# Optimization experiments

Hardware: AMD Instinct MI355X
Metric: run time of the kernel (lower is better)

The kernel has to match this reference:

```python
import jax, jax.numpy as jnp
import numpy as np

N = 100_000      # nodes
E = 1_600_000    # edges (before self-loops)
IN, OUT, HID = 64, 32, 64
BN_EPS = 1e-5

def _mlp(h, w1, b1, g, beta, w2, b2):
    # PyG MLP (num_layers=2, plain_last=True): Linear -> BatchNorm(train) -> ReLU -> Linear
    h = h @ w1 + b1
    mu = jnp.mean(h, axis=0)
    var = jnp.var(h, axis=0)
    h = (h - mu) * jax.lax.rsqrt(var + BN_EPS) * g + beta
    return jax.nn.relu(h) @ w2 + b2

def setup_inputs() -> dict:
    key = jax.random.key(0)
    ks = jax.random.split(key, 12)
    def rn(k, shape):
        fan_in = shape[0]
        return jax.random.normal(k, shape, jnp.float32) / np.sqrt(fan_in)
    x = jax.random.normal(ks[0], (N, IN), jnp.float32)
    pos = jax.random.normal(ks[1], (N, 3), jnp.float32)
    edge_index = jax.random.randint(ks[2], (2, E), 0, N, jnp.int64)
    return {
        "x": x, "pos": pos, "edge_index": edge_index,
        "w_lin": rn(ks[3], (IN, OUT)), "w_src": rn(ks[4], (IN, OUT)), "w_dst": rn(ks[5], (IN, OUT)),
        "pos_w1": rn(ks[6], (3, HID)), "pos_b1": jnp.zeros((HID,), jnp.float32),
        "pos_g": jnp.ones((HID,), jnp.float32), "pos_beta": jnp.zeros((HID,), jnp.float32),
        "pos_w2": rn(ks[7], (HID, OUT)), "pos_b2": jnp.zeros((OUT,), jnp.float32),
        "att_w1": rn(ks[8], (OUT, HID)), "att_b1": jnp.zeros((HID,), jnp.float32),
        "att_g": jnp.ones((HID,), jnp.float32), "att_beta": jnp.zeros((HID,), jnp.float32),
        "att_w2": rn(ks[9], (HID, OUT)), "att_b2": jnp.zeros((OUT,), jnp.float32),
    }

def reference(x, pos, edge_index, w_lin, w_src, w_dst,
              pos_w1, pos_b1, pos_g, pos_beta, pos_w2, pos_b2,
              att_w1, att_b1, att_g, att_beta, att_w2, att_b2):
    n = x.shape[0]
    # add self-loops (PointTransformerConv default add_self_loops=True)
    loops = jnp.arange(n, dtype=edge_index.dtype)
    src = jnp.concatenate([edge_index[0], loops])  # j (message source)
    dst = jnp.concatenate([edge_index[1], loops])  # i (message target)

    alpha_src = x @ w_src          # [N, OUT]
    alpha_dst = x @ w_dst          # [N, OUT]
    x_val = x @ w_lin              # [N, OUT]

    delta = _mlp(pos[dst] - pos[src], pos_w1, pos_b1, pos_g, pos_beta, pos_w2, pos_b2)  # [E', OUT]
    a = _mlp(alpha_dst[dst] - alpha_src[src] + delta, att_w1, att_b1, att_g, att_beta, att_w2, att_b2)

    # per-destination-node, per-channel softmax over incoming edges
    a_max = jax.ops.segment_max(a, dst, num_segments=n)           # [N, OUT]
    a = jnp.exp(a - a_max[dst])
    denom = jax.ops.segment_sum(a, dst, num_segments=n)           # [N, OUT]
    a = a / (denom[dst] + 1e-16)

    msg = a * (x_val[src] + delta)                                # [E', OUT]
    out = jax.ops.segment_sum(msg, dst, num_segments=n)           # [N, OUT]
    return out
```

## Files before the change

kernel.cpp:

```cpp
#include <hip/hip_runtime.h>

typedef unsigned int uint;
typedef unsigned short ushort;

#define BN_EPS 1e-5f

using bf16x8 = __attribute__((ext_vector_type(8))) short;
using f32x16 = __attribute__((ext_vector_type(16))) float;

union FragU { uint w[4]; bf16x8 v; };

__device__ __forceinline__ uint pk2(float lo, float hi) {
    uint r;
    asm("v_cvt_pk_bf16_f32 %0, %1, %2" : "=v"(r) : "v"(lo), "v"(hi));
    return r;
}
__device__ __forceinline__ float bfu_lo(uint u) { return __uint_as_float(u << 16); }
__device__ __forceinline__ float bfu_hi(uint u) { return __uint_as_float(u & 0xffff0000u); }

__device__ __forceinline__ void get_rowmap(int col, int* rowv) {
    FragU pa, pb;
    float c = (float)col;
    #pragma unroll
    for (int j = 0; j < 4; j++) { pa.w[j] = pk2(c, c); pb.w[j] = pk2(1.f, 1.f); }
    f32x16 d;
    #pragma unroll
    for (int r = 0; r < 16; r++) d[r] = 0.f;
    d = __builtin_amdgcn_mfma_f32_32x32x16_bf16(pa.v, pb.v, d, 0, 0, 0);
    #pragma unroll
    for (int r = 0; r < 16; r++) {
        int m = (int)(d[r] * 0.0625f + 0.5f);
        rowv[r] = (m < 0) ? 0 : (m > 31 ? 31 : m);
    }
}

template<bool SORTED>
__device__ __forceinline__ void edge_sd(int e, const int* __restrict__ ei,
                                        const int* __restrict__ srcs,
                                        const int* __restrict__ dsts,
                                        int nE, int& src, int& dst) {
    if (SORTED) { src = srcs[e]; dst = dsts[e]; }
    else if (e < nE) { src = ei[e]; dst = ei[nE + e]; }
    else { src = e - nE; dst = src; }
}

__global__ __launch_bounds__(256) void k_node_lin(
    const float* __restrict__ x,
    const float* __restrict__ w_src, const float* __restrict__ w_dst,
    const float* __restrict__ w_lin,
    uint* __restrict__ aSb, uint* __restrict__ aDb, uint* __restrict__ xvb,
    int nNodes)
{
    int n = blockIdx.x * 256 + threadIdx.x;
    if (n >= nNodes) return;
    float xr[64];
    const float4* xp = (const float4*)(x + (size_t)n * 64);
    #pragma unroll
    for (int i = 0; i < 16; i++) {
        float4 v = xp[i];
        xr[4*i] = v.x; xr[4*i+1] = v.y; xr[4*i+2] = v.z; xr[4*i+3] = v.w;
    }
    const float* ws[3] = { w_src, w_dst, w_lin };
    uint* outs[3] = { aSb, aDb, xvb };
    #pragma unroll
    for (int m = 0; m < 3; m++) {
        const float* w = ws[m];
        float acc[32];
        #pragma unroll
        for (int o = 0; o < 32; o++) acc[o] = 0.f;
        #pragma unroll
        for (int k = 0; k < 64; k++) {
            float xk = xr[k];
            #pragma unroll
            for (int o = 0; o < 32; o++) acc[o] = fmaf(xk, w[k*32+o], acc[o]);
        }
        uint4* op = (uint4*)(outs[m] + (size_t)n * 16);
        #pragma unroll
        for (int q = 0; q < 4; q++) {
            uint4 v;
            v.x = pk2(acc[8*q+0], acc[8*q+1]);
            v.y = pk2(acc[8*q+2], acc[8*q+3]);
            v.z = pk2(acc[8*q+4], acc[8*q+5]);
            v.w = pk2(acc[8*q+6], acc[8*q+7]);
            op[q] = v;
        }
    }
}

__global__ __launch_bounds__(256) void k_pos4(
    const float* __restrict__ pos, float4* __restrict__ pos4, int n)
{
    int i = blockIdx.x * 256 + threadIdx.x;
    if (i < n) pos4[i] = make_float4(pos[i*3], pos[i*3+1], pos[i*3+2], 0.f);
}

__global__ __launch_bounds__(256) void k_hist(
    const int* __restrict__ ei, int* __restrict__ cnt, int nE, int eTot)
{
    int e = blockIdx.x * 256 + threadIdx.x;
    if (e >= eTot) return;
    int dst = (e < nE) ? ei[nE + e] : (e - nE);
    atomicAdd(&cnt[dst], 1);
}

#define SCH 1024
__global__ __launch_bounds__(256) void k_scan1(
    const int* __restrict__ cnt, int* __restrict__ cur,
    int* __restrict__ blkS, int n)
{
    __shared__ int ls[256];
    int t = threadIdx.x;
    int base = blockIdx.x * SCH + t * 4;
    int v0 = (base+0 < n) ? cnt[base+0] : 0;
    int v1 = (base+1 < n) ? cnt[base+1] : 0;
    int v2 = (base+2 < n) ? cnt[base+2] : 0;
    int v3 = (base+3 < n) ? cnt[base+3] : 0;
    int tsum = v0 + v1 + v2 + v3;
    ls[t] = tsum;
    __syncthreads();
    for (int o = 1; o < 256; o <<= 1) {
        int x = (t >= o) ? ls[t-o] : 0;
        __syncthreads();
        ls[t] += x;
        __syncthreads();
    }
    if (t == 255) blkS[blockIdx.x] = ls[255];
// ... 74 lines not shown
        partM[blockIdx.x * 9 + threadIdx.x] =
            red[0][threadIdx.x] + red[1][threadIdx.x] + red[2][threadIdx.x] + red[3][threadIdx.x];
}

__global__ void k_bn1_mom(const float* __restrict__ partM, int nBlk,
                          const float* __restrict__ pw1, const float* __restrict__ pb1,
                          const float* __restrict__ g, const float* __restrict__ beta,
                          float* __restrict__ bn, float invE)
{
    __shared__ float mom_s[9];
    int l = threadIdx.x;
    #pragma unroll
    for (int c = 0; c < 9; c++) {
        float s = 0.f;
        for (int i = l; i < nBlk; i += 64) s += partM[i*9 + c];
        for (int o = 32; o > 0; o >>= 1) s += __shfl_down(s, o, 64);
        if (l == 0) mom_s[c] = s;
    }
    __syncthreads();
    int c = l;
    if (c < 64) {
        float w0 = pw1[c], w1 = pw1[64+c], w2 = pw1[128+c], b = pb1[c];
        float S = fmaf(w0, mom_s[0], fmaf(w1, mom_s[1], w2 * mom_s[2]));
        float Q = w0*w0*mom_s[3] + 2.f*w0*w1*mom_s[4] + 2.f*w0*w2*mom_s[5]
                + w1*w1*mom_s[6] + 2.f*w1*w2*mom_s[7] + w2*w2*mom_s[8];
        float mu  = S * invE + b;
        float E2  = Q * invE + 2.f * b * (S * invE) + b * b;
        float var = fmaxf(E2 - mu * mu, 0.f);
        float sc  = rsqrtf(var + BN_EPS) * g[c];
        bn[c]      = sc;
        bn[64+c]   = beta[c] - mu * sc;
    }
}

__global__ __launch_bounds__(256) void k_red_stats(
    const float* __restrict__ partD, float* __restrict__ stats2, int nBlk)
{
    int c = blockIdx.x;
    float s = 0.f;
    for (int i = threadIdx.x; i < nBlk; i += 256) s += partD[(size_t)i*128 + c];
    for (int o = 32; o > 0; o >>= 1) s += __shfl_down(s, o, 64);
    __shared__ float red[4];
    if ((threadIdx.x & 63) == 0) red[threadIdx.x >> 6] = s;
    __syncthreads();
    if (threadIdx.x == 0) stats2[c] = red[0] + red[1] + red[2] + red[3];
}

__global__ void k_bn_fin(const float* __restrict__ stats,
                         const float* __restrict__ g, const float* __restrict__ beta,
                         const float* __restrict__ bias,
                         float* __restrict__ bn, float inv_ep)
{
    int c = threadIdx.x;
    if (c < 64) {
        float b   = bias ? bias[c] : 0.f;
        float m0  = stats[c] * inv_ep;
        float mu  = m0 + b;
        float eq  = stats[64+c] * inv_ep + 2.f*b*m0 + b*b;
        float var = fmaxf(eq - mu * mu, 0.f);
        float sc  = rsqrtf(var + BN_EPS) * g[c];
        bn[c]      = sc;
        bn[64+c]   = beta[c] - mu * sc;
    }
}

__global__ void k_fold1(const float* __restrict__ pw1, const float* __restrict__ pb1,
                        const float* __restrict__ bn1,
                        float* __restrict__ pw1f, float* __restrict__ pb1f)
{
    int i = threadIdx.x;
    if (i < 192) pw1f[i] = pw1[i] * bn1[i & 63];
    if (i < 64)  pb1f[i] = pb1[i] * bn1[i] + bn1[64 + i];
}

__global__ void k_fold2(const float* __restrict__ aw1, const float* __restrict__ ab1,
                        const float* __restrict__ bn2,
                        float* __restrict__ aw1f, float* __restrict__ ab1f)
{
    int i = blockIdx.x * 256 + threadIdx.x;
    if (i < 2048) aw1f[i] = aw1[i] * bn2[i & 63];
    if (i < 64)   ab1f[i] = ab1[i] * bn2[i] + bn2[64 + i];
}

__device__ __forceinline__ void gather_row16(
    const uint* __restrict__ rowp, const int* q2, bool quadOK,
    const int* rowv, float* out)
{
    if (quadOK) {
        #pragma unroll
        for (int g = 0; g < 4; g++) {
            uint2 v = *(const uint2*)(rowp + 2*q2[g]);
            out[4*g+0] = bfu_lo(v.x);
            out[4*g+1] = bfu_hi(v.x);
            out[4*g+2] = bfu_lo(v.y);
            out[4*g+3] = bfu_hi(v.y);
        }
    } else {
        const ushort* rp = (const ushort*)rowp;
        #pragma unroll
        for (int r = 0; r < 16; r++)
            out[r] = __uint_as_float(((uint)rp[rowv[r]]) << 16);
    }
}

template<bool SORTED>
__global__ __launch_bounds__(256, 2) void k_delta_stats(
    const int* __restrict__ ei, const int* __restrict__ srcs, const int* __restrict__ dsts,
    const float4* __restrict__ pos4,
    const uint* __restrict__ aSb, const uint* __restrict__ aDb,
    const float* __restrict__ pw1f, const float* __restrict__ pb1f,
    const float* __restrict__ pw2, const float* __restrict__ pb2,
    const float* __restrict__ aw1,
    float* __restrict__ partD, int nE, int eTot)
{
    const int lane = threadIdx.x & 63;
    const int col  = lane & 31;
    const int h    = lane >> 5;

    __shared__ float redS[4][64], redQ[4][64];
    {
        int w = threadIdx.x >> 6, c = threadIdx.x & 63;
        redS[w][c] = 0.f; redQ[w][c] = 0.f;
    }

    int rowv[16];
    get_rowmap(col, rowv);
    bool quadOK = true;
    #pragma unroll
    for (int g = 0; g < 4; g++)
        quadOK = quadOK && (rowv[4*g+1] == rowv[4*g]+1)
                        && (rowv[4*g+2] == rowv[4*g]+2)
                        && (rowv[4*g+3] == rowv[4*g]+3);
    int q2[4];
    #pragma unroll
    for (int g = 0; g < 4; g++) q2[g] = rowv[4*g] >> 2;

    FragU fw_pw2[4];
    #pragma unroll
    for (int kt = 0; kt < 4; kt++)
        #pragma unroll
        for (int jw = 0; jw < 4; jw++) {
            int m = 2*jw;
            int c0 = 16*kt + 8*(m>>2) + 4*h + (m&3);
            fw_pw2[kt].w[jw] = pk2(pw2[c0*32 + col], pw2[(c0+1)*32 + col]);
        }
    FragU fw_aw1[2][2];
    #pragma unroll
    for (int mt = 0; mt < 2; mt++)
        #pragma unroll
        for (int kt = 0; kt < 2; kt++)
            #pragma unroll
            for (int jw = 0; jw < 4; jw++) {
                int u0 = rowv[8*kt + 2*jw], u1 = rowv[8*kt + 2*jw + 1];
                fw_aw1[mt][kt].w[jw] = pk2(aw1[u0*64 + 32*mt + col],
                                           aw1[u1*64 + 32*mt + col]);
            }
    float pb2v[16];
    #pragma unroll
    for (int r = 0; r < 16; r++) pb2v[r] = pb2[rowv[r]];

    float sA[32], qA[32];
    #pragma unroll
    for (int i = 0; i < 32; i++) { sA[i] = 0.f; qA[i] = 0.f; }

    const int nT = (eTot + 31) >> 5;
    const int gw = (blockIdx.x << 2) + (threadIdx.x >> 6);
    const int nW = gridDim.x << 2;
    for (int t = gw; t < nT; t += nW) {
        int e = t*32 + col;
        bool valid = e < eTot;
        int ec = valid ? e : eTot - 1;
        int src, dst;
        edge_sd<SORTED>(ec, ei, srcs, dsts, nE, src, dst);
        float4 pd = pos4[dst], ps = pos4[src];
        float p0 = pd.x - ps.x, p1 = pd.y - ps.y, p2 = pd.z - ps.z;

        FragU ft[4];
        #pragma unroll
        for (int kt = 0; kt < 4; kt++)
            #pragma unroll
            for (int mm = 0; mm < 2; mm++) {
                int cb = 16*kt + 8*mm + 4*h;
                float4 w0 = *(const float4*)(pw1f +       cb);
                float4 w1 = *(const float4*)(pw1f + 64  + cb);
                float4 w2 = *(const float4*)(pw1f + 128 + cb);
                float4 bb = *(const float4*)(pb1f + cb);
                float t0 = fmaxf(fmaf(p0,w0.x, fmaf(p1,w1.x, fmaf(p2,w2.x, bb.x))), 0.f);
                float t1 = fmaxf(fmaf(p0,w0.y, fmaf(p1,w1.y, fmaf(p2,w2.y, bb.y))), 0.f);
                float t2 = fmaxf(fmaf(p0,w0.z, fmaf(p1,w1.z, fmaf(p2,w2.z, bb.z))), 0.f);
                float t3 = fmaxf(fmaf(p0,w0.w, fmaf(p1,w1.w, fmaf(p2,w2.w, bb.w))), 0.f);
                ft[kt].w[2*mm+0] = pk2(t0, t1);
                ft[kt].w[2*mm+1] = pk2(t2, t3);
            }
        f32x16 adl;
        #pragma unroll
        for (int r = 0; r < 16; r++) adl[r] = pb2v[r];
        #pragma unroll
        for (int kt = 0; kt < 4; kt++)
            adl = __builtin_amdgcn_mfma_f32_32x32x16_bf16(fw_pw2[kt].v, ft[kt].v, adl, 0, 0, 0);

        float gD[16], gS[16];
        gather_row16(aDb + (size_t)dst*16, q2, quadOK, rowv, gD);
        gather_row16(aSb + (size_t)src*16, q2, quadOK, rowv, gS);

        FragU fu[2];
        #pragma unroll
        for (int kt = 0; kt < 2; kt++)
            #pragma unroll
            for (int jw = 0; jw < 4; jw++) {
                int r0 = 8*kt + 2*jw;
                fu[kt].w[jw] = pk2(adl[r0]   + gD[r0]   - gS[r0],
                                   adl[r0+1] + gD[r0+1] - gS[r0+1]);
            }

        f32x16 ah0, ah1;
        #pragma unroll
        for (int r = 0; r < 16; r++) { ah0[r] = 0.f; ah1[r] = 0.f; }
        #pragma unroll
        for (int kt = 0; kt < 2; kt++) {
            ah0 = __builtin_amdgcn_mfma_f32_32x32x16_bf16(fw_aw1[0][kt].v, fu[kt].v, ah0, 0, 0, 0);
            ah1 = __builtin_amdgcn_mfma_f32_32x32x16_bf16(fw_aw1[1][kt].v, fu[kt].v, ah1, 0, 0, 0);
        }
        if (valid) {
            #pragma unroll
            for (int r = 0; r < 16; r++) {
                sA[r]    += ah0[r];
                qA[r]     = fmaf(ah0[r], ah0[r], qA[r]);
                sA[16+r] += ah1[r];
                qA[16+r]  = fmaf(ah1[r], ah1[r], qA[16+r]);
            }
        }
    }
    __syncthreads();
    {
        int w = threadIdx.x >> 6;
        #pragma unroll
        for (int idx = 0; idx < 32; idx++) {
            float vs = sA[idx], vq = qA[idx];
            for (int off = 16; off > 0; off >>= 1) {
                vs += __shfl_xor(vs, off, 64);
                vq += __shfl_xor(vq, off, 64);
            }
            if ((threadIdx.x & 31) == 0) {
                int mt = idx >> 4, r = idx & 15;
                int c = 32*mt + rowv[r];
                redS[w][c] = vs;
                redQ[w][c] = vq;
            }
        }
    }
    __syncthreads();
    if (threadIdx.x < 64) {
        int c = threadIdx.x;
        float S = redS[0][c] + redS[1][c] + redS[2][c] + redS[3][c];
        float Q = redQ[0][c] + redQ[1][c] + redQ[2][c] + redQ[3][c];
        partD[(size_t)blockIdx.x*128 + c]      = S;
        partD[(size_t)blockIdx.x*128 + 64 + c] = Q;
    }
}

template<bool SORTED>
__global__ __launch_bounds__(256, 2) void k_att_agg(
    const int* __restrict__ ei, const int* __restrict__ srcs, const int* __restrict__ dsts,
    const float4* __restrict__ pos4,
    const uint* __restrict__ aSb, const uint* __restrict__ aDb,
    const uint* __restrict__ xvb,
    const float* __restrict__ pw1f, const float* __restrict__ pb1f,
    const float* __restrict__ pw2, const float* __restrict__ pb2,
    const float* __restrict__ aw1f, const float* __restrict__ ab1f,
    const float* __restrict__ aw2, const float* __restrict__ ab2,
    float* __restrict__ denom, float* __restrict__ outp,
    int nE, int eTot)
{
    const int lane = threadIdx.x & 63;
    const int col  = lane & 31;
    const int h    = lane >> 5;

    int rowv[16];
    get_rowmap(col, rowv);
    bool quadOK = true;
    #pragma unroll
    for (int g = 0; g < 4; g++)
        quadOK = quadOK && (rowv[4*g+1] == rowv[4*g]+1)
                        && (rowv[4*g+2] == rowv[4*g]+2)
                        && (rowv[4*g+3] == rowv[4*g]+3);
    int q2[4];
    #pragma unroll
    for (int g = 0; g < 4; g++) q2[g] = rowv[4*g] >> 2;

    FragU fw_pw2[4], fw_aw2[4];
    #pragma unroll
    for (int kt = 0; kt < 4; kt++)
        #pragma unroll
        for (int jw = 0; jw < 4; jw++) {
            int m = 2*jw;
            int c0 = 16*kt + 8*(m>>2) + 4*h + (m&3);
            fw_pw2[kt].w[jw] = pk2(pw2[c0*32 + col], pw2[(c0+1)*32 + col]);
            int o0 = 32*(kt>>1) + rowv[8*(kt&1) + m];
            int o1 = 32*(kt>>1) + rowv[8*(kt&1) + m + 1];
            fw_aw2[kt].w[jw] = pk2(aw2[o0*32 + col], aw2[o1*32 + col]);
        }
    FragU fw_aw1[2][2];
    #pragma unroll
    for (int mt = 0; mt < 2; mt++)
        #pragma unroll
        for (int kt = 0; kt < 2; kt++)
            #pragma unroll
            for (int jw = 0; jw < 4; jw++) {
                int u0 = rowv[8*kt + 2*jw], u1 = rowv[8*kt + 2*jw + 1];
                fw_aw1[mt][kt].w[jw] = pk2(aw1f[u0*64 + 32*mt + col],
                                           aw1f[u1*64 + 32*mt + col]);
            }
    float pb2v[16], ab2v[16], ab1v[32];
    #pragma unroll
    for (int r = 0; r < 16; r++) {
        pb2v[r]    = pb2[rowv[r]];
        ab2v[r]    = ab2[rowv[r]];
        ab1v[r]    = ab1f[rowv[r]];
        ab1v[16+r] = ab1f[32 + rowv[r]];
    }

    const int nT = (eTot + 31) >> 5;
    const int gw = (blockIdx.x << 2) + (threadIdx.x >> 6);
    const int nW = gridDim.x << 2;
    for (int t = gw; t < nT; t += nW) {
        int e = t*32 + col;
        bool valid = e < eTot;
        int ec = valid ? e : eTot - 1;
        int src, dst;
        edge_sd<SORTED>(ec, ei, srcs, dsts, nE, src, dst);
        float4 pd = pos4[dst], ps = pos4[src];
        float p0 = pd.x - ps.x, p1 = pd.y - ps.y, p2 = pd.z - ps.z;

        FragU ft[4];
        #pragma unroll
        for (int kt = 0; kt < 4; kt++)
            #pragma unroll
            for (int mm = 0; mm < 2; mm++) {
                int cb = 16*kt + 8*mm + 4*h;
                float4 w0 = *(const float4*)(pw1f +       cb);
                float4 w1 = *(const float4*)(pw1f + 64  + cb);
                float4 w2 = *(const float4*)(pw1f + 128 + cb);
                float4 bb = *(const float4*)(pb1f + cb);
                float t0 = fmaxf(fmaf(p0,w0.x, fmaf(p1,w1.x, fmaf(p2,w2.x, bb.x))), 0.f);
                float t1 = fmaxf(fmaf(p0,w0.y, fmaf(p1,w1.y, fmaf(p2,w2.y, bb.y))), 0.f);
                float t2 = fmaxf(fmaf(p0,w0.z, fmaf(p1,w1.z, fmaf(p2,w2.z, bb.z))), 0.f);
                float t3 = fmaxf(fmaf(p0,w0.w, fmaf(p1,w1.w, fmaf(p2,w2.w, bb.w))), 0.f);
                ft[kt].w[2*mm+0] = pk2(t0, t1);
                ft[kt].w[2*mm+1] = pk2(t2, t3);
            }
        f32x16 adl;
        #pragma unroll
        for (int r = 0; r < 16; r++) adl[r] = pb2v[r];
        #pragma unroll
        for (int kt = 0; kt < 4; kt++)
            adl = __builtin_amdgcn_mfma_f32_32x32x16_bf16(fw_pw2[kt].v, ft[kt].v, adl, 0, 0, 0);

        float gD[16], gS[16], xg[16];
        gather_row16(aDb + (size_t)dst*16, q2, quadOK, rowv, gD);
        gather_row16(aSb + (size_t)src*16, q2, quadOK, rowv, gS);
        gather_row16(xvb + (size_t)src*16, q2, quadOK, rowv, xg);

        FragU fu[2];
        #pragma unroll
        for (int kt = 0; kt < 2; kt++)
            #pragma unroll
            for (int jw = 0; jw < 4; jw++) {
                int r0 = 8*kt + 2*jw;
                fu[kt].w[jw] = pk2(adl[r0]   + gD[r0]   - gS[r0],
                                   adl[r0+1] + gD[r0+1] - gS[r0+1]);
            }

        f32x16 ah0, ah1;
        #pragma unroll
        for (int r = 0; r < 16; r++) { ah0[r] = ab1v[r]; ah1[r] = ab1v[16+r]; }
        #pragma unroll
        for (int kt = 0; kt < 2; kt++) {
            ah0 = __builtin_amdgcn_mfma_f32_32x32x16_bf16(fw_aw1[0][kt].v, fu[kt].v, ah0, 0, 0, 0);
            ah1 = __builtin_amdgcn_mfma_f32_32x32x16_bf16(fw_aw1[1][kt].v, fu[kt].v, ah1, 0, 0, 0);
        }
        FragU fh[4];
        #pragma unroll
        for (int q = 0; q < 4; q++)
            #pragma unroll
            for (int jw = 0; jw < 4; jw++) {
                int r0 = 8*(q&1) + 2*jw;
                float x0 = (q < 2) ? ah0[r0]   : ah1[r0];
                float x1 = (q < 2) ? ah0[r0+1] : ah1[r0+1];
                fh[q].w[jw] = pk2(fmaxf(x0, 0.f), fmaxf(x1, 0.f));
            }
        f32x16 aa;
        #pragma unroll
        for (int r = 0; r < 16; r++) aa[r] = ab2v[r];
        aa = __builtin_amdgcn_mfma_f32_32x32x16_bf16(fw_aw2[0].v, fh[0].v, aa, 0, 0, 0);
        aa = __builtin_amdgcn_mfma_f32_32x32x16_bf16(fw_aw2[1].v, fh[1].v, aa, 0, 0, 0);
        aa = __builtin_amdgcn_mfma_f32_32x32x16_bf16(fw_aw2[2].v, fh[2].v, aa, 0, 0, 0);
        aa = __builtin_amdgcn_mfma_f32_32x32x16_bf16(fw_aw2[3].v, fh[3].v, aa, 0, 0, 0);

        if (SORTED) {
            float eav[16], msv[16];
            #pragma unroll
            for (int r = 0; r < 16; r++) {
                float ea = __expf(fminf(aa[r], 35.f));
                eav[r] = valid ? ea : 0.f;
                msv[r] = valid ? ea * (xg[r] + adl[r]) : 0.f;
            }
            int lw = lane & 31;
            int dprev = __shfl_up(dst, 1, 32);
            bool isHead = (lw == 0) || (dprev != dst);
            bool eq1  = (__shfl_down(dst, 1, 32)  == dst) && (lw + 1  < 32);
            bool eq2  = (__shfl_down(dst, 2, 32)  == dst) && (lw + 2  < 32);
            bool eq4  = (__shfl_down(dst, 4, 32)  == dst) && (lw + 4  < 32);
            bool eq8  = (__shfl_down(dst, 8, 32)  == dst) && (lw + 8  < 32);
            bool eq16 = (__shfl_down(dst, 16, 32) == dst) && (lw + 16 < 32);
            float* drow = denom + (size_t)dst * 32;
            float* orow = outp  + (size_t)dst * 32;
            #pragma unroll
            for (int r = 0; r < 16; r++) {
                float ev = eav[r], mv = msv[r];
                { float a = __shfl_down(ev,1,32),  b = __shfl_down(mv,1,32);  if (eq1)  { ev += a; mv += b; } }
                { float a = __shfl_down(ev,2,32),  b = __shfl_down(mv,2,32);  if (eq2)  { ev += a; mv += b; } }
                { float a = __shfl_down(ev,4,32),  b = __shfl_down(mv,4,32);  if (eq4)  { ev += a; mv += b; } }
                { float a = __shfl_down(ev,8,32),  b = __shfl_down(mv,8,32);  if (eq8)  { ev += a; mv += b; } }
                { float a = __shfl_down(ev,16,32), b = __shfl_down(mv,16,32); if (eq16) { ev += a; mv += b; } }
                if (isHead) {
                    int o = rowv[r];
                    unsafeAtomicAdd(drow + o, ev);
                    unsafeAtomicAdd(orow + o, mv);
                }
            }
        } else if (valid) {
            float* drow = denom + (size_t)dst * 32;
            float* orow = outp  + (size_t)dst * 32;
            #pragma unroll
            for (int r = 0; r < 16; r++) {
                int o = rowv[r];
                float ea = __expf(fminf(aa[r], 35.f));
                unsafeAtomicAdd(drow + o, ea);
                unsafeAtomicAdd(orow + o, ea * (xg[r] + adl[r]));
            }
        }
    }
}

__global__ __launch_bounds__(256) void k_norm(
    float* __restrict__ out, const float* __restrict__ denom, int total)
{
    int i = blockIdx.x * 256 + threadIdx.x;
    if (i < total) out[i] = out[i] / (denom[i] + 1e-16f);
}

extern "C" void kernel_launch(void* const* d_in, const int* in_sizes, int n_in,
                              void* d_out, int out_size, void* d_ws, size_t ws_size,
                              hipStream_t stream)
{
    const float* x     = (const float*)d_in[0];
    const float* pos   = (const float*)d_in[1];
    const int*   ei    = (const int*)d_in[2];
    const float* w_lin = (const float*)d_in[3];
    const float* w_src = (const float*)d_in[4];
    const float* w_dst = (const float*)d_in[5];
    const float* pw1   = (const float*)d_in[6];
    const float* pb1   = (const float*)d_in[7];
    const float* pg    = (const float*)d_in[8];
    const float* pbeta = (const float*)d_in[9];
    const float* pw2   = (const float*)d_in[10];
    const float* pb2   = (const float*)d_in[11];
    const float* aw1   = (const float*)d_in[12];
    const float* ab1   = (const float*)d_in[13];
    const float* ag    = (const float*)d_in[14];
    const float* abeta = (const float*)d_in[15];
    const float* aw2   = (const float*)d_in[16];
    const float* ab2   = (const float*)d_in[17];
    float* out = (float*)d_out;

    const int nNodes = in_sizes[0] / 64;
    const int nE     = in_sizes[2] / 2;
    const int eTot   = nE + nNodes;

    const int PMBLK = 1024;
    const int DBLK  = 2048;

    const size_t nF = (size_t)nNodes * 32;
    uint*   aSb   = (uint*)d_ws;
    uint*   aDb   = aSb + (size_t)nNodes*16;
    uint*   xvb   = aDb + (size_t)nNodes*16;
    float*  pos4  = (float*)(xvb + (size_t)nNodes*16);
    float*  denom = pos4 + (size_t)nNodes*4;
    float*  stats = denom + nF;
    float*  bn1   = stats + 512;
    float*  bn2   = bn1 + 128;
    float*  pw1f  = bn2 + 128;
    float*  pb1f  = pw1f + 192;
    float*  aw1f  = pb1f + 64;
    float*  ab1f  = aw1f + 2048;
    float*  partM = ab1f + 64;
    float*  partD = partM + (size_t)PMBLK*9;
    float*  fend  = partD + (size_t)DBLK*128;

    int* cnt    = (int*)fend;
    int* cur    = cnt + nNodes;
    int* blkS   = cur + nNodes;
    int* blkOff = blkS + 256;
    int* srcs   = blkOff + 256;
    int* dsts   = srcs + eTot;

    size_t need_sorted = ((char*)(dsts + eTot)) - ((char*)d_ws);
    const bool sorted = ws_size >= need_sorted;

    const int nb = (nNodes + SCH - 1) / SCH;

    hipMemsetAsync(out,   0, nF * sizeof(float), stream);
    hipMemsetAsync(denom, 0, nF * sizeof(float), stream);

    k_node_lin<<<(nNodes + 255) / 256, 256, 0, stream>>>(
        x, w_src, w_dst, w_lin, aSb, aDb, xvb, nNodes);
    k_pos4<<<(nNodes + 255) / 256, 256, 0, stream>>>(pos, (float4*)pos4, nNodes);

    k_pos_mom<<<PMBLK, 256, 0, stream>>>(ei, (const float4*)pos4, partM, nE);
    k_bn1_mom<<<1, 64, 0, stream>>>(partM, PMBLK, pw1, pb1, pg, pbeta, bn1,
                                    1.0f / (float)eTot);
    k_fold1<<<1, 256, 0, stream>>>(pw1, pb1, bn1, pw1f, pb1f);
// ... 32 lines not shown
```

Before: 839.9 us.

## Software-prefetch next edge tile's indices and gathers in edge kernels

```diff
diff --git a/kernel.cpp b/kernel.cpp
--- a/kernel.cpp
+++ b/kernel.cpp
@@ -42,6 +42,60 @@
     if (SORTED) { src = srcs[e]; dst = dsts[e]; }
     else if (e < nE) { src = ei[e]; dst = ei[nE + e]; }
     else { src = e - nE; dst = src; }
+}
+
+__device__ __forceinline__ void unpack8(const uint2* gq, float* out) {
+    #pragma unroll
+    for (int g = 0; g < 4; g++) {
+        out[4*g+0] = bfu_lo(gq[g].x);
+        out[4*g+1] = bfu_hi(gq[g].x);
+        out[4*g+2] = bfu_lo(gq[g].y);
+        out[4*g+3] = bfu_hi(gq[g].y);
+    }
+}
+
+template<bool SORTED, bool WANTX>
+__device__ __forceinline__ void pref_tile(
+    int t, int col, int nE, int eTot,
+    const int* __restrict__ ei, const int* __restrict__ srcs, const int* __restrict__ dsts,
+    const float4* __restrict__ pos4,
+    const uint* __restrict__ aSb, const uint* __restrict__ xvb, const int* q2,
+    int& src, int& dst, float4& ps, float4& pd, uint2* gs, uint2* gx)
+{
+    int e = t*32 + col;
+    int ec = (e < eTot) ? e : eTot - 1;
+    edge_sd<SORTED>(ec, ei, srcs, dsts, nE, src, dst);
+    ps = pos4[src];
+    pd = pos4[dst];
+    const uint* rs = aSb + (size_t)src*16;
+    #pragma unroll
+    for (int g = 0; g < 4; g++) gs[g] = *(const uint2*)(rs + 2*q2[g]);
+    if (WANTX) {
+        const uint* rx = xvb + (size_t)src*16;
+        #pragma unroll
+        for (int g = 0; g < 4; g++) gx[g] = *(const uint2*)(rx + 2*q2[g]);
+    }
+}
+
+__device__ __forceinline__ void gather_row16(
+    const uint* __restrict__ rowp, const int* q2, bool quadOK,
+    const int* rowv, float* out)
+{
+    if (quadOK) {
+        #pragma unroll
+        for (int g = 0; g < 4; g++) {
+            uint2 v = *(const uint2*)(rowp + 2*q2[g]);
+            out[4*g+0] = bfu_lo(v.x);
+            out[4*g+1] = bfu_hi(v.x);
+            out[4*g+2] = bfu_lo(v.y);
+            out[4*g+3] = bfu_hi(v.y);
+        }
+    } else {
+        const ushort* rp = (const ushort*)rowp;
+        #pragma unroll
+        for (int r = 0; r < 16; r++)
+            out[r] = __uint_as_float(((uint)rp[rowv[r]]) << 16);
+    }
 }
 
 __global__ __launch_bounds__(256) void k_node_lin(
@@ -282,27 +336,6 @@
     if (i < 64)   ab1f[i] = ab1[i] * bn2[i] + bn2[64 + i];
 }
 
-__device__ __forceinline__ void gather_row16(
-    const uint* __restrict__ rowp, const int* q2, bool quadOK,
-    const int* rowv, float* out)
-{
-    if (quadOK) {
-        #pragma unroll
-        for (int g = 0; g < 4; g++) {
-            uint2 v = *(const uint2*)(rowp + 2*q2[g]);
-            out[4*g+0] = bfu_lo(v.x);
-            out[4*g+1] = bfu_hi(v.x);
-            out[4*g+2] = bfu_lo(v.y);
-            out[4*g+3] = bfu_hi(v.y);
-        }
-    } else {
-        const ushort* rp = (const ushort*)rowp;
-        #pragma unroll
-        for (int r = 0; r < 16; r++)
-            out[r] = __uint_as_float(((uint)rp[rowv[r]]) << 16);
-    }
-}
-
 template<bool SORTED>
 __global__ __launch_bounds__(256, 2) void k_delta_stats(
     const int* __restrict__ ei, const int* __restrict__ srcs, const int* __restrict__ dsts,
@@ -366,71 +399,152 @@
     const int nT = (eTot + 31) >> 5;
     const int gw = (blockIdx.x << 2) + (threadIdx.x >> 6);
     const int nW = gridDim.x << 2;
-    for (int t = gw; t < nT; t += nW) {
-        int e = t*32 + col;
-        bool valid = e < eTot;
-        int ec = valid ? e : eTot - 1;
-        int src, dst;
-        edge_sd<SORTED>(ec, ei, srcs, dsts, nE, src, dst);
-        float4 pd = pos4[dst], ps = pos4[src];
-        float p0 = pd.x - ps.x, p1 = pd.y - ps.y, p2 = pd.z - ps.z;
-
-        FragU ft[4];
-        #pragma unroll
-        for (int kt = 0; kt < 4; kt++)
-            #pragma unroll
-            for (int mm = 0; mm < 2; mm++) {
-                int cb = 16*kt + 8*mm + 4*h;
-                float4 w0 = *(const float4*)(pw1f +       cb);
-                float4 w1 = *(const float4*)(pw1f + 64  + cb);
-                float4 w2 = *(const float4*)(pw1f + 128 + cb);
-                float4 bb = *(const float4*)(pb1f + cb);
-                float t0 = fmaxf(fmaf(p0,w0.x, fmaf(p1,w1.x, fmaf(p2,w2.x, bb.x))), 0.f);
-                float t1 = fmaxf(fmaf(p0,w0.y, fmaf(p1,w1.y, fmaf(p2,w2.y, bb.y))), 0.f);
-                float t2 = fmaxf(fmaf(p0,w0.z, fmaf(p1,w1.z, fmaf(p2,w2.z, bb.z))), 0.f);
-                float t3 = fmaxf(fmaf(p0,w0.w, fmaf(p1,w1.w, fmaf(p2,w2.w, bb.w))), 0.f);
-                ft[kt].w[2*mm+0] = pk2(t0, t1);
-                ft[kt].w[2*mm+1] = pk2(t2, t3);
-            }
-        f32x16 adl;
-        #pragma unroll
-        for (int r = 0; r < 16; r++) adl[r] = pb2v[r];
-        #pragma unroll
-        for (int kt = 0; kt < 4; kt++)
-            adl = __builtin_amdgcn_mfma_f32_32x32x16_bf16(fw_pw2[kt].v, ft[kt].v, adl, 0, 0, 0);
-
-        float gD[16], gS[16];
-        gather_row16(aDb + (size_t)dst*16, q2, quadOK, rowv, gD);
-        gather_row16(aSb + (size_t)src*16, q2, quadOK, rowv, gS);
-
-        FragU fu[2];
-        #pragma unroll
-        for (int kt = 0; kt < 2; kt++)
-            #pragma unroll
-            for (int jw = 0; jw < 4; jw++) {
-                int r0 = 8*kt + 2*jw;
-                fu[kt].w[jw] = pk2(adl[r0]   + gD[r0]   - gS[r0],
-                                   adl[r0+1] + gD[r0+1] - gS[r0+1]);
-            }
-
-        f32x16 ah0, ah1;
-        #pragma unroll
-        for (int r = 0; r < 16; r++) { ah0[r] = 0.f; ah1[r] = 0.f; }
-        #pragma unroll
-        for (int kt = 0; kt < 2; kt++) {
-            ah0 = __builtin_amdgcn_mfma_f32_32x32x16_bf16(fw_aw1[0][kt].v, fu[kt].v, ah0, 0, 0, 0);
-            ah1 = __builtin_amdgcn_mfma_f32_32x32x16_bf16(fw_aw1[1][kt].v, fu[kt].v, ah1, 0, 0, 0);
+
+    if (quadOK) {
+        int c_src, c_dst; float4 c_ps, c_pd; uint2 c_gs[4], c_gx[4];
+        int t = gw;
+        if (t < nT)
+            pref_tile<SORTED, false>(t, col, nE, eTot, ei, srcs, dsts, pos4,
+                                     aSb, nullptr, q2, c_src, c_dst, c_ps, c_pd, c_gs, c_gx);
+        for (; t < nT; ) {
+            int tn = t + nW;
+            int tc = (tn < nT) ? tn : t;
+            int n_src, n_dst; float4 n_ps, n_pd; uint2 n_gs[4], n_gx[4];
+            pref_tile<SORTED, false>(tc, col, nE, eTot, ei, srcs, dsts, pos4,
+                                     aSb, nullptr, q2, n_src, n_dst, n_ps, n_pd, n_gs, n_gx);
+            bool valid = (t*32 + col) < eTot;
+            uint2 gd2[4];
+            {
+                const uint* rd = aDb + (size_t)c_dst*16;
+                #pragma unroll
+                for (int g = 0; g < 4; g++) gd2[g] = *(const uint2*)(rd + 2*q2[g]);
+            }
+            float p0 = c_pd.x - c_ps.x, p1 = c_pd.y - c_ps.y, p2 = c_pd.z - c_ps.z;
+
+            FragU ft[4];
+            #pragma unroll
+            for (int kt = 0; kt < 4; kt++)
+                #pragma unroll
+                for (int mm = 0; mm < 2; mm++) {
+                    int cb = 16*kt + 8*mm + 4*h;
+                    float4 w0 = *(const float4*)(pw1f +       cb);
+                    float4 w1 = *(const float4*)(pw1f + 64  + cb);
+                    float4 w2 = *(const float4*)(pw1f + 128 + cb);
+                    float4 bb = *(const float4*)(pb1f + cb);
+                    float t0 = fmaxf(fmaf(p0,w0.x, fmaf(p1,w1.x, fmaf(p2,w2.x, bb.x))), 0.f);
+                    float t1 = fmaxf(fmaf(p0,w0.y, fmaf(p1,w1.y, fmaf(p2,w2.y, bb.y))), 0.f);
+                    float t2 = fmaxf(fmaf(p0,w0.z, fmaf(p1,w1.z, fmaf(p2,w2.z, bb.z))), 0.f);
+                    float t3 = fmaxf(fmaf(p0,w0.w, fmaf(p1,w1.w, fmaf(p2,w2.w, bb.w))), 0.f);
+                    ft[kt].w[2*mm+0] = pk2(t0, t1);
+                    ft[kt].w[2*mm+1] = pk2(t2, t3);
+                }
+            f32x16 adl;
+            #pragma unroll
+            for (int r = 0; r < 16; r++) adl[r] = pb2v[r];
+            #pragma unroll
+            for (int kt = 0; kt < 4; kt++)
+                adl = __builtin_amdgcn_mfma_f32_32x32x16_bf16(fw_pw2[kt].v, ft[kt].v, adl, 0, 0, 0);
+
+            float gD[16], gS[16];
+            unpack8(gd2, gD);
+            unpack8(c_gs, gS);
+
+            FragU fu[2];
+            #pragma unroll
+            for (int kt = 0; kt < 2; kt++)
+                #pragma unroll
+                for (int jw = 0; jw < 4; jw++) {
+                    int r0 = 8*kt + 2*jw;
+                    fu[kt].w[jw] = pk2(adl[r0]   + gD[r0]   - gS[r0],
+                                       adl[r0+1] + gD[r0+1] - gS[r0+1]);
+                }
+
+            f32x16 ah0, ah1;
+            #pragma unroll
+            for (int r = 0; r < 16; r++) { ah0[r] = 0.f; ah1[r] = 0.f; }
+            #pragma unroll
+            for (int kt = 0; kt < 2; kt++) {
+                ah0 = __builtin_amdgcn_mfma_f32_32x32x16_bf16(fw_aw1[0][kt].v, fu[kt].v, ah0, 0, 0, 0);
+                ah1 = __builtin_amdgcn_mfma_f32_32x32x16_bf16(fw_aw1[1][kt].v, fu[kt].v, ah1, 0, 0, 0);
+            }
+            if (valid) {
+                #pragma unroll
+                for (int r = 0; r < 16; r++) {
+                    sA[r]    += ah0[r];
+                    qA[r]     = fmaf(ah0[r], ah0[r], qA[r]);
+                    sA[16+r] += ah1[r];
+                    qA[16+r]  = fmaf(ah1[r], ah1[r], qA[16+r]);
+                }
+            }
+            c_src = n_src; c_dst = n_dst; c_ps = n_ps; c_pd = n_pd;
+            #pragma unroll
+            for (int g = 0; g < 4; g++) c_gs[g] = n_gs[g];
+            t = tn;
         }
-        if (valid) {
-            #pragma unroll
-            for (int r = 0; r < 16; r++) {
-                sA[r]    += ah0[r];
-                qA[r]     = fmaf(ah0[r], ah0[r], qA[r]);
-                sA[16+r] += ah1[r];
-                qA[16+r]  = fmaf(ah1[r], ah1[r], qA[16+r]);
+    } else {
+        for (int t = gw; t < nT; t += nW) {
+            int e = t*32 + col;
+            bool valid = e < eTot;
+            int ec = valid ? e : eTot - 1;
+            int src, dst;
+            edge_sd<SORTED>(ec, ei, srcs, dsts, nE, src, dst);
+            float4 pd = pos4[dst], ps = pos4[src];
+            float p0 = pd.x - ps.x, p1 = pd.y - ps.y, p2 = pd.z - ps.z;
+            FragU ft[4];
+            #pragma unroll
+            for (int kt = 0; kt < 4; kt++)
+                #pragma unroll
+                for (int mm = 0; mm < 2; mm++) {
+                    int cb = 16*kt + 8*mm + 4*h;
+                    float4 w0 = *(const float4*)(pw1f +       cb);
+                    float4 w1 = *(const float4*)(pw1f + 64  + cb);
+                    float4 w2 = *(const float4*)(pw1f + 128 + cb);
+                    float4 bb = *(const float4*)(pb1f + cb);
+                    float t0 = fmaxf(fmaf(p0,w0.x, fmaf(p1,w1.x, fmaf(p2,w2.x, bb.x))), 0.f);
+                    float t1 = fmaxf(fmaf(p0,w0.y, fmaf(p1,w1.y, fmaf(p2,w2.y, bb.y))), 0.f);
+                    float t2 = fmaxf(fmaf(p0,w0.z, fmaf(p1,w1.z, fmaf(p2,w2.z, bb.z))), 0.f);
+                    float t3 = fmaxf(fmaf(p0,w0.w, fmaf(p1,w1.w, fmaf(p2,w2.w, bb.w))), 0.f);
+                    ft[kt].w[2*mm+0] = pk2(t0, t1);
+                    ft[kt].w[2*mm+1] = pk2(t2, t3);
+                }
+            f32x16 adl;
+            #pragma unroll
+            for (int r = 0; r < 16; r++) adl[r] = pb2v[r];
+            #pragma unroll
+            for (int kt = 0; kt < 4; kt++)
+                adl = __builtin_amdgcn_mfma_f32_32x32x16_bf16(fw_pw2[kt].v, ft[kt].v, adl, 0, 0, 0);
+            float gD[16], gS[16];
+            gather_row16(aDb + (size_t)dst*16, q2, false, rowv, gD);
+            gather_row16(aSb + (size_t)src*16, q2, false, rowv, gS);
+            FragU fu[2];
+            #pragma unroll
+            for (int kt = 0; kt < 2; kt++)
+                #pragma unroll
+                for (int jw = 0; jw < 4; jw++) {
+                    int r0 = 8*kt + 2*jw;
+                    fu[kt].w[jw] = pk2(adl[r0]   + gD[r0]   - gS[r0],
+                                       adl[r0+1] + gD[r0+1] - gS[r0+1]);
+                }
+            f32x16 ah0, ah1;
+            #pragma unroll
+            for (int r = 0; r < 16; r++) { ah0[r] = 0.f; ah1[r] = 0.f; }
+            #pragma unroll
+            for (int kt = 0; kt < 2; kt++) {
+                ah0 = __builtin_amdgcn_mfma_f32_32x32x16_bf16(fw_aw1[0][kt].v, fu[kt].v, ah0, 0, 0, 0);
+                ah1 = __builtin_amdgcn_mfma_f32_32x32x16_bf16(fw_aw1[1][kt].v, fu[kt].v, ah1, 0, 0, 0);
+            }
+            if (valid) {
+                #pragma unroll
+                for (int r = 0; r < 16; r++) {
+                    sA[r]    += ah0[r];
+                    qA[r]     = fmaf(ah0[r], ah0[r], qA[r]);
+                    sA[16+r] += ah1[r];
+                    qA[16+r]  = fmaf(ah1[r], ah1[r], qA[16+r]);
+                }
             }
         }
     }
+
     __syncthreads();
     {
         int w = threadIdx.x >> 6;
@@ -523,121 +637,254 @@
     const int nT = (eTot + 31) >> 5;
     const int gw = (blockIdx.x << 2) + (threadIdx.x >> 6);
     const int nW = gridDim.x << 2;
-    for (int t = gw; t < nT; t += nW) {
-        int e = t*32 + col;
-        bool valid = e < eTot;
-        int ec = valid ? e : eTot - 1;
-        int src, dst;
-        edge_sd<SORTED>(ec, ei, srcs, dsts, nE, src, dst);
-        float4 pd = pos4[dst], ps = pos4[src];
-        float p0 = pd.x - ps.x, p1 = pd.y - ps.y, p2 = pd.z - ps.z;
-
-        FragU ft[4];
-        #pragma unroll
-        for (int kt = 0; kt < 4; kt++)
-            #pragma unroll
-            for (int mm = 0; mm < 2; mm++) {
-                int cb = 16*kt + 8*mm + 4*h;
-                float4 w0 = *(const float4*)(pw1f +       cb);
-                float4 w1 = *(const float4*)(pw1f + 64  + cb);
-                float4 w2 = *(const float4*)(pw1f + 128 + cb);
-                float4 bb = *(const float4*)(pb1f + cb);
-                float t0 = fmaxf(fmaf(p0,w0.x, fmaf(p1,w1.x, fmaf(p2,w2.x, bb.x))), 0.f);
-                float t1 = fmaxf(fmaf(p0,w0.y, fmaf(p1,w1.y, fmaf(p2,w2.y, bb.y))), 0.f);
-                float t2 = fmaxf(fmaf(p0,w0.z, fmaf(p1,w1.z, fmaf(p2,w2.z, bb.z))), 0.f);
-                float t3 = fmaxf(fmaf(p0,w0.w, fmaf(p1,w1.w, fmaf(p2,w2.w, bb.w))), 0.f);
-                ft[kt].w[2*mm+0] = pk2(t0, t1);
-                ft[kt].w[2*mm+1] = pk2(t2, t3);
-            }
-        f32x16 adl;
-        #pragma unroll
-        for (int r = 0; r < 16; r++) adl[r] = pb2v[r];
-        #pragma unroll
-        for (int kt = 0; kt < 4; kt++)
-            adl = __builtin_amdgcn_mfma_f32_32x32x16_bf16(fw_pw2[kt].v, ft[kt].v, adl, 0, 0, 0);
-
-        float gD[16], gS[16], xg[16];
-        gather_row16(aDb + (size_t)dst*16, q2, quadOK, rowv, gD);
-        gather_row16(aSb + (size_t)src*16, q2, quadOK, rowv, gS);
-        gather_row16(xvb + (size_t)src*16, q2, quadOK, rowv, xg);
-
-        FragU fu[2];
-        #pragma unroll
-        for (int kt = 0; kt < 2; kt++)
-            #pragma unroll
-            for (int jw = 0; jw < 4; jw++) {
-                int r0 = 8*kt + 2*jw;
-                fu[kt].w[jw] = pk2(adl[r0]   + gD[r0]   - gS[r0],
-                                   adl[r0+1] + gD[r0+1] - gS[r0+1]);
-            }
-
-        f32x16 ah0, ah1;
-        #pragma unroll
-        for (int r = 0; r < 16; r++) { ah0[r] = ab1v[r]; ah1[r] = ab1v[16+r]; }
-        #pragma unroll
-        for (int kt = 0; kt < 2; kt++) {
-            ah0 = __builtin_amdgcn_mfma_f32_32x32x16_bf16(fw_aw1[0][kt].v, fu[kt].v, ah0, 0, 0, 0);
-            ah1 = __builtin_amdgcn_mfma_f32_32x32x16_bf16(fw_aw1[1][kt].v, fu[kt].v, ah1, 0, 0, 0);
+
+    if (quadOK) {
+        int c_src, c_dst; float4 c_ps, c_pd; uint2 c_gs[4], c_gx[4];
+        int t = gw;
+        if (t < nT)
+            pref_tile<SORTED, true>(t, col, nE, eTot, ei, srcs, dsts, pos4,
+                                    aSb, xvb, q2, c_src, c_dst, c_ps, c_pd, c_gs, c_gx);
+        for (; t < nT; ) {
+            int tn = t + nW;
+            int tc = (tn < nT) ? tn : t;
+            int n_src, n_dst; float4 n_ps, n_pd; uint2 n_gs[4], n_gx[4];
+            pref_tile<SORTED, true>(tc, col, nE, eTot, ei, srcs, dsts, pos4,
+                                    aSb, xvb, q2, n_src, n_dst, n_ps, n_pd, n_gs, n_gx);
+            bool valid = (t*32 + col) < eTot;
+            int dst = c_dst;
+            uint2 gd2[4];
+            {
+                const uint* rd = aDb + (size_t)dst*16;
+                #pragma unroll
+                for (int g = 0; g < 4; g++) gd2[g] = *(const uint2*)(rd + 2*q2[g]);
+            }
+            float p0 = c_pd.x - c_ps.x, p1 = c_pd.y - c_ps.y, p2 = c_pd.z - c_ps.z;
+
+            FragU ft[4];
+            #pragma unroll
+            for (int kt = 0; kt < 4; kt++)
+                #pragma unroll
+                for (int mm = 0; mm < 2; mm++) {
+                    int cb = 16*kt + 8*mm + 4*h;
+                    float4 w0 = *(const float4*)(pw1f +       cb);
+                    float4 w1 = *(const float4*)(pw1f + 64  + cb);
+                    float4 w2 = *(const float4*)(pw1f + 128 + cb);
+                    float4 bb = *(const float4*)(pb1f + cb);
+                    float t0 = fmaxf(fmaf(p0,w0.x, fmaf(p1,w1.x, fmaf(p2,w2.x, bb.x))), 0.f);
+                    float t1 = fmaxf(fmaf(p0,w0.y, fmaf(p1,w1.y, fmaf(p2,w2.y, bb.y))), 0.f);
+                    float t2 = fmaxf(fmaf(p0,w0.z, fmaf(p1,w1.z, fmaf(p2,w2.z, bb.z))), 0.f);
+                    float t3 = fmaxf(fmaf(p0,w0.w, fmaf(p1,w1.w, fmaf(p2,w2.w, bb.w))), 0.f);
+                    ft[kt].w[2*mm+0] = pk2(t0, t1);
+                    ft[kt].w[2*mm+1] = pk2(t2, t3);
+                }
+            f32x16 adl;
+            #pragma unroll
+            for (int r = 0; r < 16; r++) adl[r] = pb2v[r];
+            #pragma unroll
+            for (int kt = 0; kt < 4; kt++)
+                adl = __builtin_amdgcn_mfma_f32_32x32x16_bf16(fw_pw2[kt].v, ft[kt].v, adl, 0, 0, 0);
+
+            float gD[16], gS[16], xg[16];
+            unpack8(gd2, gD);
+            unpack8(c_gs, gS);
+            unpack8(c_gx, xg);
+
+            FragU fu[2];
+            #pragma unroll
+            for (int kt = 0; kt < 2; kt++)
+                #pragma unroll
+                for (int jw = 0; jw < 4; jw++) {
+                    int r0 = 8*kt + 2*jw;
+                    fu[kt].w[jw] = pk2(adl[r0]   + gD[r0]   - gS[r0],
+                                       adl[r0+1] + gD[r0+1] - gS[r0+1]);
+                }
+
+            f32x16 ah0, ah1;
+            #pragma unroll
+            for (int r = 0; r < 16; r++) { ah0[r] = ab1v[r]; ah1[r] = ab1v[16+r]; }
+            #pragma unroll
+            for (int kt = 0; kt < 2; kt++) {
+                ah0 = __builtin_amdgcn_mfma_f32_32x32x16_bf16(fw_aw1[0][kt].v, fu[kt].v, ah0, 0, 0, 0);
+                ah1 = __builtin_amdgcn_mfma_f32_32x32x16_bf16(fw_aw1[1][kt].v, fu[kt].v, ah1, 0, 0, 0);
+            }
+            FragU fh[4];
+            #pragma unroll
+            for (int q = 0; q < 4; q++)
+                #pragma unroll
+                for (int jw = 0; jw < 4; jw++) {
+                    int r0 = 8*(q&1) + 2*jw;
+                    float x0 = (q < 2) ? ah0[r0]   : ah1[r0];
+                    float x1 = (q < 2) ? ah0[r0+1] : ah1[r0+1];
+                    fh[q].w[jw] = pk2(fmaxf(x0, 0.f), fmaxf(x1, 0.f));
+                }
+            f32x16 aa;
+            #pragma unroll
+            for (int r = 0; r < 16; r++) aa[r] = ab2v[r];
+            aa = __builtin_amdgcn_mfma_f32_32x32x16_bf16(fw_aw2[0].v, fh[0].v, aa, 0, 0, 0);
+            aa = __builtin_amdgcn_mfma_f32_32x32x16_bf16(fw_aw2[1].v, fh[1].v, aa, 0, 0, 0);
+            aa = __builtin_amdgcn_mfma_f32_32x32x16_bf16(fw_aw2[2].v, fh[2].v, aa, 0, 0, 0);
+            aa = __builtin_amdgcn_mfma_f32_32x32x16_bf16(fw_aw2[3].v, fh[3].v, aa, 0, 0, 0);
+
+            if (SORTED) {
+                float eav[16], msv[16];
+                #pragma unroll
+                for (int r = 0; r < 16; r++) {
+                    float ea = __expf(fminf(aa[r], 35.f));
+                    eav[r] = valid ? ea : 0.f;
+                    msv[r] = valid ? ea * (xg[r] + adl[r]) : 0.f;
+                }
+                int lw = lane & 31;
+                int dprev = __shfl_up(dst, 1, 32);
+                bool isHead = (lw == 0) || (dprev != dst);
+                bool eq1  = (__shfl_down(dst, 1, 32)  == dst) && (lw + 1  < 32);
+                bool eq2  = (__shfl_down(dst, 2, 32)  == dst) && (lw + 2  < 32);
+                bool eq4  = (__shfl_down(dst, 4, 32)  == dst) && (lw + 4  < 32);
+                bool eq8  = (__shfl_down(dst, 8, 32)  == dst) && (lw + 8  < 32);
+                bool eq16 = (__shfl_down(dst, 16, 32) == dst) && (lw + 16 < 32);
+                float* drow = denom + (size_t)dst * 32;
+                float* orow = outp  + (size_t)dst * 32;
+                #pragma unroll
+                for (int r = 0; r < 16; r++) {
+                    float ev = eav[r], mv = msv[r];
+                    { float a = __shfl_down(ev,1,32),  b = __shfl_down(mv,1,32);  if (eq1)  { ev += a; mv += b; } }
+                    { float a = __shfl_down(ev,2,32),  b = __shfl_down(mv,2,32);  if (eq2)  { ev += a; mv += b; } }
+                    { float a = __shfl_down(ev,4,32),  b = __shfl_down(mv,4,32);  if (eq4)  { ev += a; mv += b; } }
+                    { float a = __shfl_down(ev,8,32),  b = __shfl_down(mv,8,32);  if (eq8)  { ev += a; mv += b; } }
+                    { float a = __shfl_down(ev,16,32), b = __shfl_down(mv,16,32); if (eq16) { ev += a; mv += b; } }
+                    if (isHead) {
+                        int o = rowv[r];
+                        unsafeAtomicAdd(drow + o, ev);
+                        unsafeAtomicAdd(orow + o, mv);
+                    }
+                }
+            } else if (valid) {
+                float* drow = denom + (size_t)dst * 32;
+                float* orow = outp  + (size_t)dst * 32;
+                #pragma unroll
+                for (int r = 0; r < 16; r++) {
+                    int o = rowv[r];
+                    float ea = __expf(fminf(aa[r], 35.f));
+                    unsafeAtomicAdd(drow + o, ea);
+                    unsafeAtomicAdd(orow + o, ea * (xg[r] + adl[r]));
+                }
+            }
+            c_src = n_src; c_dst = n_dst; c_ps = n_ps; c_pd = n_pd;
+            #pragma unroll
+            for (int g = 0; g < 4; g++) { c_gs[g] = n_gs[g]; c_gx[g] = n_gx[g]; }
+            t = tn;
         }
-        FragU fh[4];
-        #pragma unroll
-        for (int q = 0; q < 4; q++)
-            #pragma unroll
-            for (int jw = 0; jw < 4; jw++) {
-                int r0 = 8*(q&1) + 2*jw;
-                float x0 = (q < 2) ? ah0[r0]   : ah1[r0];
-                float x1 = (q < 2) ? ah0[r0+1] : ah1[r0+1];
-                fh[q].w[jw] = pk2(fmaxf(x0, 0.f), fmaxf(x1, 0.f));
-            }
-        f32x16 aa;
-        #pragma unroll
-        for (int r = 0; r < 16; r++) aa[r] = ab2v[r];
-        aa = __builtin_amdgcn_mfma_f32_32x32x16_bf16(fw_aw2[0].v, fh[0].v, aa, 0, 0, 0);
-        aa = __builtin_amdgcn_mfma_f32_32x32x16_bf16(fw_aw2[1].v, fh[1].v, aa, 0, 0, 0);
-        aa = __builtin_amdgcn_mfma_f32_32x32x16_bf16(fw_aw2[2].v, fh[2].v, aa, 0, 0, 0);
-        aa = __builtin_amdgcn_mfma_f32_32x32x16_bf16(fw_aw2[3].v, fh[3].v, aa, 0, 0, 0);
-
-        if (SORTED) {
-            float eav[16], msv[16];
-            #pragma unroll
-            for (int r = 0; r < 16; r++) {
-                float ea = __expf(fminf(aa[r], 35.f));
-                eav[r] = valid ? ea : 0.f;
-                msv[r] = valid ? ea * (xg[r] + adl[r]) : 0.f;
-            }
-            int lw = lane & 31;
-            int dprev = __shfl_up(dst, 1, 32);
-            bool isHead = (lw == 0) || (dprev != dst);
-            bool eq1  = (__shfl_down(dst, 1, 32)  == dst) && (lw + 1  < 32);
-            bool eq2  = (__shfl_down(dst, 2, 32)  == dst) && (lw + 2  < 32);
-            bool eq4  = (__shfl_down(dst, 4, 32)  == dst) && (lw + 4  < 32);
-            bool eq8  = (__shfl_down(dst, 8, 32)  == dst) && (lw + 8  < 32);
-            bool eq16 = (__shfl_down(dst, 16, 32) == dst) && (lw + 16 < 32);
-            float* drow = denom + (size_t)dst * 32;
-            float* orow = outp  + (size_t)dst * 32;
-            #pragma unroll
-            for (int r = 0; r < 16; r++) {
-                float ev = eav[r], mv = msv[r];
-                { float a = __shfl_down(ev,1,32),  b = __shfl_down(mv,1,32);  if (eq1)  { ev += a; mv += b; } }
-                { float a = __shfl_down(ev,2,32),  b = __shfl_down(mv,2,32);  if (eq2)  { ev += a; mv += b; } }
-                { float a = __shfl_down(ev,4,32),  b = __shfl_down(mv,4,32);  if (eq4)  { ev += a; mv += b; } }
-                { float a = __shfl_down(ev,8,32),  b = __shfl_down(mv,8,32);  if (eq8)  { ev += a; mv += b; } }
-                { float a = __shfl_down(ev,16,32), b = __shfl_down(mv,16,32); if (eq16) { ev += a; mv += b; } }
-                if (isHead) {
+    } else {
+        for (int t = gw; t < nT; t += nW) {
+            int e = t*32 + col;
+            bool valid = e < eTot;
+            int ec = valid ? e : eTot - 1;
+            int src, dst;
+            edge_sd<SORTED>(ec, ei, srcs, dsts, nE, src, dst);
+            float4 pd = pos4[dst], ps = pos4[src];
+            float p0 = pd.x - ps.x, p1 = pd.y - ps.y, p2 = pd.z - ps.z;
+            FragU ft[4];
+            #pragma unroll
+            for (int kt = 0; kt < 4; kt++)
+                #pragma unroll
+                for (int mm = 0; mm < 2; mm++) {
+                    int cb = 16*kt + 8*mm + 4*h;
+                    float4 w0 = *(const float4*)(pw1f +       cb);
+                    float4 w1 = *(const float4*)(pw1f + 64  + cb);
+                    float4 w2 = *(const float4*)(pw1f + 128 + cb);
+                    float4 bb = *(const float4*)(pb1f + cb);
+                    float t0 = fmaxf(fmaf(p0,w0.x, fmaf(p1,w1.x, fmaf(p2,w2.x, bb.x))), 0.f);
+                    float t1 = fmaxf(fmaf(p0,w0.y, fmaf(p1,w1.y, fmaf(p2,w2.y, bb.y))), 0.f);
+                    float t2 = fmaxf(fmaf(p0,w0.z, fmaf(p1,w1.z, fmaf(p2,w2.z, bb.z))), 0.f);
+                    float t3 = fmaxf(fmaf(p0,w0.w, fmaf(p1,w1.w, fmaf(p2,w2.w, bb.w))), 0.f);
+                    ft[kt].w[2*mm+0] = pk2(t0, t1);
+                    ft[kt].w[2*mm+1] = pk2(t2, t3);
+                }
+            f32x16 adl;
+            #pragma unroll
+            for (int r = 0; r < 16; r++) adl[r] = pb2v[r];
+            #pragma unroll
+            for (int kt = 0; kt < 4; kt++)
+                adl = __builtin_amdgcn_mfma_f32_32x32x16_bf16(fw_pw2[kt].v, ft[kt].v, adl, 0, 0, 0);
+            float gD[16], gS[16], xg[16];
+            gather_row16(aDb + (size_t)dst*16, q2, false, rowv, gD);
+            gather_row16(aSb + (size_t)src*16, q2, false, rowv, gS);
+            gather_row16(xvb + (size_t)src*16, q2, false, rowv, xg);
+            FragU fu[2];
+            #pragma unroll
+            for (int kt = 0; kt < 2; kt++)
+                #pragma unroll
+                for (int jw = 0; jw < 4; jw++) {
+                    int r0 = 8*kt + 2*jw;
+                    fu[kt].w[jw] = pk2(adl[r0]   + gD[r0]   - gS[r0],
+                                       adl[r0+1] + gD[r0+1] - gS[r0+1]);
+                }
+            f32x16 ah0, ah1;
+            #pragma unroll
+            for (int r = 0; r < 16; r++) { ah0[r] = ab1v[r]; ah1[r] = ab1v[16+r]; }
+            #pragma unroll
+            for (int kt = 0; kt < 2; kt++) {
+                ah0 = __builtin_amdgcn_mfma_f32_32x32x16_bf16(fw_aw1[0][kt].v, fu[kt].v, ah0, 0, 0, 0);
+                ah1 = __builtin_amdgcn_mfma_f32_32x32x16_bf16(fw_aw1[1][kt].v, fu[kt].v, ah1, 0, 0, 0);
+            }
+            FragU fh[4];
+            #pragma unroll
+            for (int q = 0; q < 4; q++)
+                #pragma unroll
+                for (int jw = 0; jw < 4; jw++) {
+                    int r0 = 8*(q&1) + 2*jw;
+                    float x0 = (q < 2) ? ah0[r0]   : ah1[r0];
+                    float x1 = (q < 2) ? ah0[r0+1] : ah1[r0+1];
+                    fh[q].w[jw] = pk2(fmaxf(x0, 0.f), fmaxf(x1, 0.f));
+                }
+            f32x16 aa;
+            #pragma unroll
+            for (int r = 0; r < 16; r++) aa[r] = ab2v[r];
+            aa = __builtin_amdgcn_mfma_f32_32x32x16_bf16(fw_aw2[0].v, fh[0].v, aa, 0, 0, 0);
+            aa = __builtin_amdgcn_mfma_f32_32x32x16_bf16(fw_aw2[1].v, fh[1].v, aa, 0, 0, 0);
+            aa = __builtin_amdgcn_mfma_f32_32x32x16_bf16(fw_aw2[2].v, fh[2].v, aa, 0, 0, 0);
+            aa = __builtin_amdgcn_mfma_f32_32x32x16_bf16(fw_aw2[3].v, fh[3].v, aa, 0, 0, 0);
+            if (SORTED) {
+                float eav[16], msv[16];
+                #pragma unroll
+                for (int r = 0; r < 16; r++) {
+                    float ea = __expf(fminf(aa[r], 35.f));
+                    eav[r] = valid ? ea : 0.f;
+                    msv[r] = valid ? ea * (xg[r] + adl[r]) : 0.f;
+                }
+                int lw = lane & 31;
+                int dprev = __shfl_up(dst, 1, 32);
+                bool isHead = (lw == 0) || (dprev != dst);
+                bool eq1  = (__shfl_down(dst, 1, 32)  == dst) && (lw + 1  < 32);
+                bool eq2  = (__shfl_down(dst, 2, 32)  == dst) && (lw + 2  < 32);
+                bool eq4  = (__shfl_down(dst, 4, 32)  == dst) && (lw + 4  < 32);
+                bool eq8  = (__shfl_down(dst, 8, 32)  == dst) && (lw + 8  < 32);
+                bool eq16 = (__shfl_down(dst, 16, 32) == dst) && (lw + 16 < 32);
+                float* drow = denom + (size_t)dst * 32;
+                float* orow = outp  + (size_t)dst * 32;
+                #pragma unroll
+                for (int r = 0; r < 16; r++) {
+                    float ev = eav[r], mv = msv[r];
+                    { float a = __shfl_down(ev,1,32),  b = __shfl_down(mv,1,32);  if (eq1)  { ev += a; mv += b; } }
+                    { float a = __shfl_down(ev,2,32),  b = __shfl_down(mv,2,32);  if (eq2)  { ev += a; mv += b; } }
+                    { float a = __shfl_down(ev,4,32),  b = __shfl_down(mv,4,32);  if (eq4)  { ev += a; mv += b; } }
+                    { float a = __shfl_down(ev,8,32),  b = __shfl_down(mv,8,32);  if (eq8)  { ev += a; mv += b; } }
+                    { float a = __shfl_down(ev,16,32), b = __shfl_down(mv,16,32); if (eq16) { ev += a; mv += b; } }
+                    if (isHead) {
+                        int o = rowv[r];
+                        unsafeAtomicAdd(drow + o, ev);
+                        unsafeAtomicAdd(orow + o, mv);
+                    }
+                }
+            } else if (valid) {
+                float* drow = denom + (size_t)dst * 32;
+                float* orow = outp  + (size_t)dst * 32;
+                #pragma unroll
+                for (int r = 0; r < 16; r++) {
                     int o = rowv[r];
-                    unsafeAtomicAdd(drow + o, ev);
-                    unsafeAtomicAdd(orow + o, mv);
-                }
-            }
-        } else if (valid) {
-            float* drow = denom + (size_t)dst * 32;
-            float* orow = outp  + (size_t)dst * 32;
-            #pragma unroll
-            for (int r = 0; r < 16; r++) {
-                int o = rowv[r];
-                float ea = __expf(fminf(aa[r], 35.f));
-                unsafeAtomicAdd(drow + o, ea);
-                unsafeAtomicAdd(orow + o, ea * (xg[r] + adl[r]));
+                    float ea = __expf(fminf(aa[r], 35.f));
+                    unsafeAtomicAdd(drow + o, ea);
+                    unsafeAtomicAdd(orow + o, ea * (xg[r] + adl[r]));
+                }
             }
         }
     }
```

New measurement: 827.8 us. No clear change (-1.4%).
